# Optimization experiments

Hardware: AMD Instinct MI355X
Metric: run time of the kernel (lower is better)

The kernel has to match this reference:

```python
import jax, jax.numpy as jnp
import numpy as np

B, S, E, H, L, A = 4, 4096, 512, 8, 4, 3
NV, TD = 16, 6
WIN = 64
D = E // H
NEG = -1e9


def layer_norm(x, s, b):
    m = jnp.mean(x, axis=-1, keepdims=True)
    v = jnp.mean((x - m) ** 2, axis=-1, keepdims=True)
    return (x - m) * jax.lax.rsqrt(v + 1e-5) * s + b


def kmeans_attention(x, mask, Wq, Wk, Wv, Wo, means):
    # scatter-mean results back to sequence positions.
    b, n, e = x.shape
    split = lambda t: t.reshape(b, n, H, D).transpose(0, 2, 1, 3)  # (b,h,n,d)
    q, k, v = split(x @ Wq), split(x @ Wk), split(x @ Wv)
    qn = q / (jnp.linalg.norm(q, axis=-1, keepdims=True) + 1e-8)
    mn = means / (jnp.linalg.norm(means, axis=-1, keepdims=True) + 1e-8)
    dists = jnp.einsum('bhnd,hcd->bhcn', qn, mn)          # (b,h,C,n)
    _, idx = jax.lax.top_k(dists, WIN)                    # (b,h,C,w) token ids per cluster
    c = idx.shape[2]
    gather = lambda t: jnp.take_along_axis(t[:, :, None], idx[..., None], axis=3)
    qb, kb, vb = gather(q), gather(k), gather(v)          # (b,h,C,w,d)
    km = jnp.take_along_axis(jnp.broadcast_to(mask[:, None, None, :], (b, H, c, n)), idx, axis=3)
    scores = jnp.einsum('bhcwd,bhcxd->bhcwx', qb, kb) * (D ** -0.5)
    allowed = (idx[..., :, None] >= idx[..., None, :]) & km[..., None, :]
    attn = jax.nn.softmax(jnp.where(allowed, scores, NEG), axis=-1)
    ob = jnp.einsum('bhcwx,bhcxd->bhcwd', attn, vb)
    fi = idx.reshape(b, H, c * WIN)
    fo = ob.reshape(b, H, c * WIN, D)
    bi = jnp.arange(b)[:, None, None]
    hi = jnp.arange(H)[None, :, None]
    out = jnp.zeros((b, H, n, D), x.dtype).at[bi, hi, fi].add(fo)
    cnt = jnp.zeros((b, H, n), x.dtype).at[bi, hi, fi].add(1.0)
    out = out / jnp.maximum(cnt, 1.0)[..., None]          # scatter-mean
    return out.transpose(0, 2, 1, 3).reshape(b, n, e) @ Wo


def setup_inputs():
    key = jax.random.key(0)
    ks = jax.random.split(key, 20)
    w = lambda k, shp, s=0.02: jax.random.normal(k, shp, dtype=jnp.float32) * s
    return {
        'value': jax.random.randint(ks[0], (B, S), 0, NV + 1),
        'depth': jax.random.randint(ks[1], (B, S), 0, TD + 1),
        'pos': jax.random.randint(ks[2], (B, S, A), 0, 2 ** TD + 1),
        'sos': w(ks[3], (E,), 1.0),
        'tok_emb': w(ks[4], (NV + 1, E), 1.0).at[0].set(0.0),      # padding_idx=0
        'depth_emb': w(ks[5], (TD + 1, E), 1.0).at[0].set(0.0),
        'pos_emb': w(ks[6], (A, 2 ** TD + 1, E), 1.0).at[:, 0].set(0.0),
        'ln1_s': jnp.ones((L, E), jnp.float32),
        'ln1_b': jnp.zeros((L, E), jnp.float32),
        'Wq': w(ks[7], (L, E, E)),
        'Wk': w(ks[8], (L, E, E)),
        'Wv': w(ks[9], (L, E, E)),
        'Wo': w(ks[10], (L, E, E)),
        'means': w(ks[11], (L, H, S // WIN, D), 1.0),
        'ln2_s': jnp.ones((L, E), jnp.float32),
        'ln2_b': jnp.zeros((L, E), jnp.float32),
        'W1': w(ks[12], (L, E, 4 * E)),
        'b1': jnp.zeros((L, 4 * E), jnp.float32),
        'W2': w(ks[13], (L, 4 * E, E)),
        'b2': jnp.zeros((L, E), jnp.float32),
        'head_w': w(ks[14], (NV + 1, E)),
    }


def reference(value, depth, pos, sos, tok_emb, depth_emb, pos_emb, ln1_s, ln1_b, Wq, Wk, Wv, Wo, means, ln2_s, ln2_b, W1, b1, W2, b2, head_w):
    mask = value != 0
    x = tok_emb[value] + depth_emb[depth]
    for a in range(A):
        x = x + pos_emb[a][pos[:, :, a]]
    # shift right with learned sos token
    x = jnp.concatenate([jnp.broadcast_to(sos, (B, 1, E)), x[:, :-1]], axis=1)
    for l in range(L):
        h = layer_norm(x, ln1_s[l], ln1_b[l])
        x = x + kmeans_attention(h, mask, Wq[l], Wk[l], Wv[l], Wo[l], means[l])
        h = layer_norm(x, ln2_s[l], ln2_b[l])
        x = x + (jax.nn.gelu(h @ W1[l] + b1[l]) @ W2[l] + b2[l])
    return x @ head_w.T
```

## Files before the change

### kernel.cpp

```cpp
#include <hip/hip_runtime.h>
#include <hip/hip_bf16.h>
#include <math.h>

typedef __hip_bfloat16 bf16;
typedef __attribute__((ext_vector_type(2))) float f2v;
typedef __attribute__((ext_vector_type(8))) short bf16x8;
typedef __attribute__((ext_vector_type(4))) float f32x4;

#define NB 4
#define NS 4096
#define NE 512
#define NH 8
#define NL 4
#define NA 3
#define ND 64
#define NC 64
#define NW 64
#define NF 2048
#define NVOC 17
#define NTOK (NB * NS)

__device__ __forceinline__ float b2f(bf16 v) { return __bfloat162float(v); }
__device__ __forceinline__ float u2f(unsigned short u) { return __uint_as_float((unsigned)u << 16); }
__device__ __forceinline__ float ldw(const void* p, size_t i, int f32) {
  return f32 ? ((const float*)p)[i] : b2f(((const bf16*)p)[i]);
}
__device__ __forceinline__ unsigned short f2bf(float f) {
  unsigned u = __float_as_uint(f);
  return (unsigned short)((u + 0x7FFFu + ((u >> 16) & 1u)) >> 16);
}
__device__ __forceinline__ void split3(float a, unsigned short& h, unsigned short& m,
                                       unsigned short& l) {
  h = f2bf(a);
  float r = a - u2f(h);
  m = f2bf(r);
  float s = r - u2f(m);
  l = f2bf(s);
}

__global__ __launch_bounds__(256) void fill_out_kernel(float* __restrict__ out, int n, float val) {
  int i = blockIdx.x * 256 + threadIdx.x;
  if (i < n) out[i] = val;
}

__global__ __launch_bounds__(256) void zero_kernel(float* __restrict__ p, int n) {
  int i = blockIdx.x * 256 + threadIdx.x;
  if (i < n) p[i] = 0.f;
}

__global__ __launch_bounds__(256) void embed_kernel(
    const int* __restrict__ value, const int* __restrict__ depth, const int* __restrict__ pos,
    const void* __restrict__ sos, const void* __restrict__ tok_emb,
    const void* __restrict__ depth_emb, const void* __restrict__ pos_emb,
    float* __restrict__ x, int f32) {
  int i = blockIdx.x * 256 + threadIdx.x;
  if (i >= NTOK * NE) return;
  int e = i & (NE - 1);
  int bs = i >> 9;
  int s = bs & (NS - 1);
  int b = bs >> 12;
  float v;
  if (s == 0) {
    v = ldw(sos, e, f32);
  } else {
    int src = b * NS + (s - 1);
    float acc = ldw(tok_emb, (size_t)value[src] * NE + e, f32)
              + ldw(depth_emb, (size_t)depth[src] * NE + e, f32);
#pragma unroll
    for (int a = 0; a < NA; a++)
      acc += ldw(pos_emb, ((size_t)a * 65 + pos[src * NA + a]) * NE + e, f32);
    v = acc;
  }
  x[i] = v;
}

__global__ __launch_bounds__(256) void ln_kernel(
    const float* __restrict__ x, const void* __restrict__ gam, const void* __restrict__ bet,
    size_t off, float* __restrict__ out, int f32) {
  int row = blockIdx.x * 4 + (threadIdx.x >> 6);
  int lane = threadIdx.x & 63;
  const float* xr = x + (size_t)row * NE;
  float v[8];
#pragma unroll
  for (int i = 0; i < 8; i++) v[i] = xr[lane + i * 64];
  float s = 0.f;
#pragma unroll
  for (int i = 0; i < 8; i++) s += v[i];
#pragma unroll
  for (int o = 32; o; o >>= 1) s += __shfl_xor(s, o);
  float m = s * (1.0f / NE);
  float sq = 0.f;
#pragma unroll
  for (int i = 0; i < 8; i++) { float d = v[i] - m; sq += d * d; }
#pragma unroll
  for (int o = 32; o; o >>= 1) sq += __shfl_xor(sq, o);
  float rs = 1.0f / sqrtf(sq * (1.0f / NE) + 1e-5f);
  float* orow = out + (size_t)row * NE;
#pragma unroll
  for (int i = 0; i < 8; i++) {
    int e = lane + i * 64;
    orow[e] = (v[i] - m) * rs * ldw(gam, off + e, f32) + ldw(bet, off + e, f32);
  }
}

template <int ACT>
__device__ __forceinline__ void gemm_body(
    const float* __restrict__ A, const void* __restrict__ Bw, size_t bwoff, int ldb,
    const void* bias, size_t biasoff, const float* resid, float* C,
    int N, int K, int f32, int bm, int bn) {
  __shared__ float As[32][132];
  __shared__ float Bs[32][132];
  int tid = threadIdx.x;
  int ty = tid >> 4, tx = tid & 15;
  f2v acc2[8][4];
#pragma unroll
  for (int i = 0; i < 8; i++)
#pragma unroll
    for (int j = 0; j < 4; j++) acc2[i][j] = (f2v){0.f, 0.f};
  int arow = tid >> 1;
  int acol = (tid & 1) << 4;
  int brow = tid >> 3;
  int bcol = (tid & 7) << 4;

  const float* Aptr = A + (size_t)(bm + arow) * K + acol;
  float4 pa[4];
  float4 pb[4];
  uint4 pbu[2];
#pragma unroll
  for (int j = 0; j < 4; j++) pa[j] = *(const float4*)(Aptr + 4 * j);
  {
    size_t boff = bwoff + (size_t)brow * ldb + bn + bcol;
    if (f32) {
#pragma unroll
      for (int j = 0; j < 4; j++) pb[j] = *(const float4*)((const float*)Bw + boff + 4 * j);
    } else {
      pbu[0] = *(const uint4*)((const bf16*)Bw + boff);
      pbu[1] = *(const uint4*)((const bf16*)Bw + boff + 8);
    }
  }

  for (int k0 = 0; k0 < K; k0 += 32) {
#pragma unroll
    for (int j = 0; j < 4; j++) {
      As[acol + 4 * j + 0][arow] = pa[j].x;
      As[acol + 4 * j + 1][arow] = pa[j].y;
      As[acol + 4 * j + 2][arow] = pa[j].z;
      As[acol + 4 * j + 3][arow] = pa[j].w;
    }
    if (f32) {
#pragma unroll
      for (int j = 0; j < 4; j++) {
        Bs[brow][bcol + 4 * j + 0] = pb[j].x;
        Bs[brow][bcol + 4 * j + 1] = pb[j].y;
        Bs[brow][bcol + 4 * j + 2] = pb[j].z;
        Bs[brow][bcol + 4 * j + 3] = pb[j].w;
      }
    } else {
      union { uint4 u; unsigned short s[8]; } r0, r1;
      r0.u = pbu[0]; r1.u = pbu[1];
#pragma unroll
      for (int j = 0; j < 8; j++) Bs[brow][bcol + j] = u2f(r0.s[j]);
#pragma unroll
      for (int j = 0; j < 8; j++) Bs[brow][bcol + 8 + j] = u2f(r1.s[j]);
    }
    __syncthreads();
    if (k0 + 32 < K) {
#pragma unroll
      for (int j = 0; j < 4; j++) pa[j] = *(const float4*)(Aptr + k0 + 32 + 4 * j);
      size_t boff = bwoff + (size_t)(k0 + 32 + brow) * ldb + bn + bcol;
      if (f32) {
#pragma unroll
        for (int j = 0; j < 4; j++) pb[j] = *(const float4*)((const float*)Bw + boff + 4 * j);
      } else {
        pbu[0] = *(const uint4*)((const bf16*)Bw + boff);
        pbu[1] = *(const uint4*)((const bf16*)Bw + boff + 8);
      }
    }
#pragma unroll
    for (int kk = 0; kk < 32; kk++) {
      float4 aA = *(const float4*)&As[kk][ty << 3];
      float4 aB = *(const float4*)&As[kk][(ty << 3) + 4];
      float4 bA = *(const float4*)&Bs[kk][tx << 2];
      float4 bB = *(const float4*)&Bs[kk][64 + (tx << 2)];
      float av[8] = {aA.x, aA.y, aA.z, aA.w, aB.x, aB.y, aB.z, aB.w};
      f2v bv[4];
      bv[0] = (f2v){bA.x, bA.y};
      bv[1] = (f2v){bA.z, bA.w};
      bv[2] = (f2v){bB.x, bB.y};
      bv[3] = (f2v){bB.z, bB.w};
#pragma unroll
      for (int i = 0; i < 8; i++)
#pragma unroll
        for (int j = 0; j < 4; j++)
          acc2[i][j] += bv[j] * av[i];
    }
    __syncthreads();
  }
#pragma unroll
  for (int i = 0; i < 8; i++) {
    int row = bm + (ty << 3) + i;
    int c0 = bn + (tx << 2);
    int c1 = bn + 64 + (tx << 2);
    const float* ap = (const float*)&acc2[i][0];
    float o0[4], o1[4];
#pragma unroll
    for (int j = 0; j < 4; j++) { o0[j] = ap[j]; o1[j] = ap[4 + j]; }
    if (bias) {
#pragma unroll
      for (int j = 0; j < 4; j++) {
        o0[j] += ldw(bias, biasoff + c0 + j, f32);
        o1[j] += ldw(bias, biasoff + c1 + j, f32);
      }
    }
    if (ACT == 1) {
#pragma unroll
      for (int j = 0; j < 4; j++) {
        float t0 = 0.7978845608028654f * (o0[j] + 0.044715f * o0[j] * o0[j] * o0[j]);
        o0[j] = 0.5f * o0[j] * (1.0f + tanhf(t0));
        float t1 = 0.7978845608028654f * (o1[j] + 0.044715f * o1[j] * o1[j] * o1[j]);
        o1[j] = 0.5f * o1[j] * (1.0f + tanhf(t1));
      }
    }
    size_t p0 = (size_t)row * N + c0;
    size_t p1 = (size_t)row * N + c1;
    if (resid) {
      float4 r0 = *(const float4*)(resid + p0);
      float4 r1 = *(const float4*)(resid + p1);
      o0[0] += r0.x; o0[1] += r0.y; o0[2] += r0.z; o0[3] += r0.w;
      o1[0] += r1.x; o1[1] += r1.y; o1[2] += r1.z; o1[3] += r1.w;
    }
    *(float4*)(C + p0) = make_float4(o0[0], o0[1], o0[2], o0[3]);
    *(float4*)(C + p1) = make_float4(o1[0], o1[1], o1[2], o1[3]);
  }
}

template <int ACT>
__global__ __launch_bounds__(256) void gemm_kernel(
    const float* __restrict__ A, const void* __restrict__ Bw, size_t bwoff, int ldb,
    const void* bias, size_t biasoff, const float* resid, float* C,
    int N, int K, int f32) {
  gemm_body<ACT>(A, Bw, bwoff, ldb, bias, biasoff, resid, C, N, K,
                 f32, blockIdx.y << 7, blockIdx.x << 7);
}

__global__ __launch_bounds__(256) void gemm_qkv_kernel(
    const float* __restrict__ A,
    const void* __restrict__ Wq, const void* __restrict__ Wk, const void* __restrict__ Wv,
    size_t bwoff, float* __restrict__ Cq, float* __restrict__ Ck, float* __restrict__ Cv,
    int f32) {
  int sel = blockIdx.x >> 2;
  const void* Bw = (sel == 0) ? Wq : ((sel == 1) ? Wk : Wv);
  float* C = (sel == 0) ? Cq : ((sel == 1) ? Ck : Cv);
  gemm_body<0>(A, Bw, bwoff, NE, nullptr, 0, nullptr, C, NE, NE,
               f32, blockIdx.y << 7, (blockIdx.x & 3) << 7);
}

template <int ACT, int FULL>
__device__ __forceinline__ void mfma_body(
    const float* __restrict__ A, const float* __restrict__ Bw, int ldb,
    const float* __restrict__ bias, const float* __restrict__ resid, float* __restrict__ C,
    int N, int K, int bm, int bn) {
  __shared__ unsigned short Ah[128][40];
  __shared__ unsigned short Am[128][40];
  __shared__ unsigned short Al[FULL ? 128 : 1][40];
  __shared__ unsigned short Bh[128][40];
  __shared__ unsigned short Bm[128][40];
  __shared__ unsigned short Bl[FULL ? 128 : 1][40];
  int t = threadIdx.x;
  int arow = t >> 1;
  int akc = (t & 1) << 4;
  const float* Ap = A + (size_t)(bm + arow) * K + akc;
  int bkr = t >> 3;
  int bcg = t & 7;
  const float* Bp = Bw + (size_t)bkr * ldb + bn + bcg * 16;
  int bkpos = bkr ^ ((bcg & 3) << 3);

  float4 pa[4], pb[4];
#pragma unroll
  for (int j = 0; j < 4; j++) pa[j] = *(const float4*)(Ap + 4 * j);
#pragma unroll
  for (int j = 0; j < 4; j++) pb[j] = *(const float4*)(Bp + 4 * j);

  int lane = t & 63;
  int wid = t >> 6;
  int wr = wid >> 1, wc = wid & 1;
  int lr = lane & 15, lg = lane >> 4;

  f32x4 acc[4][4];
#pragma unroll
  for (int i = 0; i < 4; i++)
#pragma unroll
    for (int j = 0; j < 4; j++) acc[i][j] = (f32x4){0.f, 0.f, 0.f, 0.f};

  for (int k0 = 0; k0 < K; k0 += 32) {
    {
      unsigned hs[8], ms[8], ls[8];
#pragma unroll
      for (int j = 0; j < 4; j++) {
        const float* pf = (const float*)&pa[j];
#pragma unroll
        for (int e = 0; e < 2; e++) {
          float a0 = pf[2 * e], a1 = pf[2 * e + 1];
          unsigned short h0 = f2bf(a0), h1 = f2bf(a1);
          float r0 = a0 - u2f(h0), r1 = a1 - u2f(h1);
          unsigned short m0 = f2bf(r0), m1 = f2bf(r1);
          hs[2 * j + e] = (unsigned)h0 | ((unsigned)h1 << 16);
          ms[2 * j + e] = (unsigned)m0 | ((unsigned)m1 << 16);
          if (FULL) {
            float s0 = r0 - u2f(m0), s1 = r1 - u2f(m1);
            unsigned short l0 = f2bf(s0), l1 = f2bf(s1);
            ls[2 * j + e] = (unsigned)l0 | ((unsigned)l1 << 16);
          }
        }
      }
      *(uint4*)&Ah[arow][akc]     = make_uint4(hs[0], hs[1], hs[2], hs[3]);
      *(uint4*)&Ah[arow][akc + 8] = make_uint4(hs[4], hs[5], hs[6], hs[7]);
      *(uint4*)&Am[arow][akc]     = make_uint4(ms[0], ms[1], ms[2], ms[3]);
      *(uint4*)&Am[arow][akc + 8] = make_uint4(ms[4], ms[5], ms[6], ms[7]);
      if (FULL) {
        *(uint4*)&Al[arow][akc]     = make_uint4(ls[0], ls[1], ls[2], ls[3]);
        *(uint4*)&Al[arow][akc + 8] = make_uint4(ls[4], ls[5], ls[6], ls[7]);
      }
    }
    {
#pragma unroll
      for (int j = 0; j < 4; j++) {
        const float* pf = (const float*)&pb[j];
#pragma unroll
        for (int e = 0; e < 4; e++) {
          float a = pf[e];
          unsigned short h = f2bf(a);
          float r = a - u2f(h);
          unsigned short m = f2bf(r);
          int nn = bcg * 16 + 4 * j + e;
          Bh[nn][bkpos] = h;
          Bm[nn][bkpos] = m;
          if (FULL) {
            float s = r - u2f(m);
            Bl[nn][bkpos] = f2bf(s);
          }
        }
      }
    }
    __syncthreads();
    if (k0 + 32 < K) {
#pragma unroll
      for (int j = 0; j < 4; j++) pa[j] = *(const float4*)(Ap + k0 + 32 + 4 * j);
      const float* Bn = Bp + (size_t)(k0 + 32) * ldb;
#pragma unroll
      for (int j = 0; j < 4; j++) pb[j] = *(const float4*)(Bn + 4 * j);
    }
    bf16x8 fbh[4], fbm[4], fbl[4];
#pragma unroll
    for (int ni = 0; ni < 4; ni++) {
      int rb = wc * 64 + ni * 16 + lr;
      int cb = ((lg ^ ni) & 3) * 8;
      fbh[ni] = *(const bf16x8*)&Bh[rb][cb];
      fbm[ni] = *(const bf16x8*)&Bm[rb][cb];
      if (FULL) fbl[ni] = *(const bf16x8*)&Bl[rb][cb];
    }
#pragma unroll
    for (int mi = 0; mi < 4; mi++) {
      int ar = wr * 64 + mi * 16 + lr;
      bf16x8 fh = *(const bf16x8*)&Ah[ar][lg * 8];
      bf16x8 fm = *(const bf16x8*)&Am[ar][lg * 8];
      bf16x8 fl;
      if (FULL) fl = *(const bf16x8*)&Al[ar][lg * 8];
#pragma unroll
      for (int ni = 0; ni < 4; ni++) {
        f32x4 a = acc[mi][ni];
        a = __builtin_amdgcn_mfma_f32_16x16x32_bf16(fh, fbh[ni], a, 0, 0, 0);
        a = __builtin_amdgcn_mfma_f32_16x16x32_bf16(fh, fbm[ni], a, 0, 0, 0);
        a = __builtin_amdgcn_mfma_f32_16x16x32_bf16(fm, fbh[ni], a, 0, 0, 0);
        if (FULL) {
          a = __builtin_amdgcn_mfma_f32_16x16x32_bf16(fm, fbm[ni], a, 0, 0, 0);
          a = __builtin_amdgcn_mfma_f32_16x16x32_bf16(fh, fbl[ni], a, 0, 0, 0);
          a = __builtin_amdgcn_mfma_f32_16x16x32_bf16(fl, fbh[ni], a, 0, 0, 0);
        }
        acc[mi][ni] = a;
      }
    }
    __syncthreads();
  }
#pragma unroll
  for (int mi = 0; mi < 4; mi++) {
#pragma unroll
    for (int ni = 0; ni < 4; ni++) {
      int col = bn + wc * 64 + ni * 16 + lr;
      int rbase = bm + wr * 64 + mi * 16 + lg * 4;
      float bv = bias ? bias[col] : 0.f;
      const float* av = (const float*)&acc[mi][ni];
#pragma unroll
      for (int r = 0; r < 4; r++) {
        float o = av[r] + bv;
        if (ACT == 1) {
          float t0 = 0.7978845608028654f * (o + 0.044715f * o * o * o);
          o = 0.5f * o * (1.0f + tanhf(t0));
        }
        size_t p = (size_t)(rbase + r) * N + col;
        if (resid) o += resid[p];
        C[p] = o;
      }
    }
  }
}

template <int ACT, int FULL>
__global__ __launch_bounds__(256) void gemm_mfma_kernel(
    const float* __restrict__ A, const float* __restrict__ Bw, int ldb,
    const float* __restrict__ bias, const float* __restrict__ resid, float* __restrict__ C,
    int N, int K) {
  mfma_body<ACT, FULL>(A, Bw, ldb, bias, resid, C, N, K, blockIdx.y << 7, blockIdx.x << 7);
}

__global__ __launch_bounds__(256) void gemm_kv_mfma(
    const float* __restrict__ A, const float* __restrict__ Wk, const float* __restrict__ Wv,
    size_t off, float* __restrict__ Ck, float* __restrict__ Cv) {
  int sel = blockIdx.x >> 2;
  const float* Bw = sel ? Wv : Wk;
  float* C = sel ? Cv : Ck;
  mfma_body<0, 0>(A, Bw + off, NE, nullptr, nullptr, C, NE, NE,
                  blockIdx.y << 7, (blockIdx.x & 3) << 7);
}

__global__ __launch_bounds__(256) void qt_kernel(const float* __restrict__ q, float* __restrict__ qT,
                                                 double* __restrict__ rqd) {
  __shared__ float tile[64][65];
  int bid = blockIdx.x;
  int st = bid & 63;
  int bh = bid >> 6;
  int b = bh >> 3, h = bh & 7;
  int s0 = st * 64;
  int t = threadIdx.x;
#pragma unroll
  for (int k = 0; k < 16; k++) {
    int idx = t + k * 256;
    int sl = idx >> 6, dl = idx & 63;
    tile[sl][dl] = q[(size_t)(b * NS + s0 + sl) * NE + h * ND + dl];
  }
  __syncthreads();
#pragma unroll
  for (int k = 0; k < 16; k++) {
    int idx = t + k * 256;
    int dl = idx >> 6, sl = idx & 63;
    qT[((size_t)bh * 64 + dl) * NS + s0 + sl] = tile[sl][dl];
  }
  int w = t >> 6, lane = t & 63;
#pragma unroll
  for (int i = 0; i < 16; i++) {
    int tok = w * 16 + i;
    double v = (double)tile[tok][lane];
    double ss = v * v;
#pragma unroll
    for (int o = 32; o; o >>= 1) ss += __shfl_xor(ss, o);
    if (lane == 0) rqd[((size_t)bh << 12) | (s0 + tok)] = 1.0 / (sqrt(ss) + 1e-8);
  }
}

__global__ __launch_bounds__(64) void mnd_kernel(const void* __restrict__ means,
                                                 double* __restrict__ mnd, int f32) {
  __shared__ double s[64];
  int vblk = blockIdx.x;
  int d = threadIdx.x;
  double m = (double)ldw(means, (size_t)vblk * ND + d, f32);
  s[d] = m * m;
  __syncthreads();
  for (int st = 32; st; st >>= 1) { if (d < st) s[d] += s[d + st]; __syncthreads(); }
  mnd[(size_t)vblk * ND + d] = m / (sqrt(s[0]) + 1e-8);
}

__global__ __launch_bounds__(256) void route_kernel(
    const float* __restrict__ qT, const double* __restrict__ mnd,
    const double* __restrict__ rqd, int* __restrict__ idxout, float* __restrict__ cnt) {
  __shared__ unsigned long long keys[NS];
  __shared__ double mc[ND];
  __shared__ unsigned hist[256];
  __shared__ unsigned short cand[2][NS];
  __shared__ unsigned s_rem, s_cnt, s_sel, s_cc[2];
  int bid = blockIdx.x;
  int h = bid & 7;
  int b = (bid >> 3) & 3;
  int c = bid >> 5;
  int bhc = ((b * NH + h) * NC) + c;
  int t = threadIdx.x;
  if (t < ND) mc[t] = mnd[((size_t)h * NC + c) * ND + t];
  hist[t] = 0u;
  if (t == 0) { s_rem = NW; s_cnt = 0u; s_cc[0] = 0u; s_cc[1] = 0u; }
  __syncthreads();
  const float* qTb = qT + (size_t)(b * NH + h) * 64 * NS;
  const double* rqb = rqd + ((size_t)(b * NH + h) << 12);
  for (int i = 0; i < 16; i += 4) {
    int n0 = t + i * 256, n1 = n0 + 256, n2 = n0 + 512, n3 = n0 + 768;
    double a0 = 0.0, a1 = 0.0, a2 = 0.0, a3 = 0.0;
#pragma unroll 8
    for (int d = 0; d < 64; d++) {
      const float* row = qTb + (size_t)d * NS;
      double m = mc[d];
      a0 += (double)row[n0] * m;
      a1 += (double)row[n1] * m;
      a2 += (double)row[n2] * m;
      a3 += (double)row[n3] * m;
    }
    double dv[4] = {a0 * rqb[n0], a1 * rqb[n1], a2 * rqb[n2], a3 * rqb[n3]};
    int nn[4] = {n0, n1, n2, n3};
#pragma unroll
    for (int j = 0; j < 4; j++) {
      long long sb = __double_as_longlong(dv[j]);
      unsigned long long u = (unsigned long long)sb;
      u = (sb < 0) ? ~u : (u | 0x8000000000000000ULL);
      keys[nn[j]] = (u & 0xFFFFFFFFFFFFF000ULL) | (unsigned long long)(NS - 1 - nn[j]);
    }
  }
  __syncthreads();
  {
    unsigned lastd = 0xFFFFFFFFu, lcnt = 0u;
    for (int n = t; n < NS; n += 256) {
      unsigned d = (unsigned)(keys[n] >> 56);
      if (d == lastd) { lcnt++; }
      else { if (lcnt) atomicAdd(&hist[lastd], lcnt); lastd = d; lcnt = 1u; }
    }
    if (lcnt) atomicAdd(&hist[lastd], lcnt);
  }
  __syncthreads();
  if (t < 64) {
    unsigned h0 = hist[4 * t + 0], h1 = hist[4 * t + 1];
    unsigned h2 = hist[4 * t + 2], h3 = hist[4 * t + 3];
    hist[4 * t + 0] = 0u; hist[4 * t + 1] = 0u; hist[4 * t + 2] = 0u; hist[4 * t + 3] = 0u;
    unsigned t3 = h3, t2 = h2 + h3, t1 = h1 + t2, t0 = h0 + t1;
    unsigned s = t0;
#pragma unroll
    for (int off = 1; off < 64; off <<= 1) {
      unsigned v = __shfl_down(s, off);
      if (t + off < 64) s += v;
    }
    unsigned E = s - t0;
    unsigned rem = s_rem;
    unsigned sf0 = t0 + E, sf1 = t1 + E, sf2 = t2 + E, sf3 = t3 + E, sf4 = E;
    if (sf0 >= rem && sf1 < rem) { s_sel = 4u * t + 0u; s_rem = rem - sf1; }
    if (sf1 >= rem && sf2 < rem) { s_sel = 4u * t + 1u; s_rem = rem - sf2; }
    if (sf2 >= rem && sf3 < rem) { s_sel = 4u * t + 2u; s_rem = rem - sf3; }
    if (sf3 >= rem && sf4 < rem) { s_sel = 4u * t + 3u; s_rem = rem - sf4; }
  }
  __syncthreads();
  {
    unsigned sel = s_sel;
    for (int n = t; n < NS; n += 256) {
      unsigned d = (unsigned)(keys[n] >> 56);
      if (d > sel) {
        unsigned p = atomicAdd(&s_cnt, 1u);
        idxout[(size_t)bhc * NW + p] = n;
        atomicAdd(&cnt[(size_t)(b * NS + n) * NH + h], 1.0f);
      } else if (d == sel) {
        unsigned p = atomicAdd(&s_cc[0], 1u);
        cand[0][p] = (unsigned short)n;
      }
    }
  }
  __syncthreads();
  int cur = 0;
  for (int p = 6; p >= 0; p--) {
    int sh = p * 8;
    unsigned nc = s_cc[cur];
    for (unsigned i = t; i < nc; i += 256) {
      unsigned d = (unsigned)((keys[cand[cur][i]] >> sh) & 255ULL);
      atomicAdd(&hist[d], 1u);
    }
    __syncthreads();
    if (t < 64) {
      unsigned h0 = hist[4 * t + 0], h1 = hist[4 * t + 1];
      unsigned h2 = hist[4 * t + 2], h3 = hist[4 * t + 3];
      hist[4 * t + 0] = 0u; hist[4 * t + 1] = 0u; hist[4 * t + 2] = 0u; hist[4 * t + 3] = 0u;
      unsigned t3 = h3, t2 = h2 + h3, t1 = h1 + t2, t0 = h0 + t1;
      unsigned s = t0;
#pragma unroll
      for (int off = 1; off < 64; off <<= 1) {
        unsigned v = __shfl_down(s, off);
        if (t + off < 64) s += v;
      }
      unsigned E = s - t0;
      unsigned rem = s_rem;
      unsigned sf0 = t0 + E, sf1 = t1 + E, sf2 = t2 + E, sf3 = t3 + E, sf4 = E;
      if (sf0 >= rem && sf1 < rem) { s_sel = 4u * t + 0u; s_rem = rem - sf1; }
      if (sf1 >= rem && sf2 < rem) { s_sel = 4u * t + 1u; s_rem = rem - sf2; }
      if (sf2 >= rem && sf3 < rem) { s_sel = 4u * t + 2u; s_rem = rem - sf3; }
      if (sf3 >= rem && sf4 < rem) { s_sel = 4u * t + 3u; s_rem = rem - sf4; }
      if (t == 0) s_cc[cur ^ 1] = 0u;
    }
    __syncthreads();
    unsigned sel = s_sel;
    if (p == 0) {
      for (unsigned i = t; i < nc; i += 256) {
        unsigned n = cand[cur][i];
        unsigned d = (unsigned)(keys[n] & 255ULL);
        if (d >= sel) {
          unsigned pp = atomicAdd(&s_cnt, 1u);
          idxout[(size_t)bhc * NW + pp] = n;
          atomicAdd(&cnt[(size_t)(b * NS + n) * NH + h], 1.0f);
        }
      }
    } else {
      int nxt = cur ^ 1;
      for (unsigned i = t; i < nc; i += 256) {
        unsigned n = cand[cur][i];
        unsigned d = (unsigned)((keys[n] >> sh) & 255ULL);
        if (d > sel) {
          unsigned pp = atomicAdd(&s_cnt, 1u);
          idxout[(size_t)bhc * NW + pp] = n;
          atomicAdd(&cnt[(size_t)(b * NS + n) * NH + h], 1.0f);
        } else if (d == sel) {
          unsigned pp = atomicAdd(&s_cc[nxt], 1u);
          cand[nxt][pp] = (unsigned short)n;
        }
      }
      __syncthreads();
      cur = nxt;
    }
  }
}

__global__ __launch_bounds__(256) void attn_kernel(
    const float* __restrict__ q, const float* __restrict__ k, const float* __restrict__ v,
    const int* __restrict__ idxb, const int* __restrict__ value, const float* __restrict__ cnt,
    float* __restrict__ obuf) {
  __shared__ float qs[NW * (ND + 1)];
  __shared__ float ks[NW * (ND + 1)];
  __shared__ float sc[NW * (NW + 1)];
  __shared__ int idxs[NW];
  __shared__ float kmv[NW];
  __shared__ float cinv[NW];
  int bhc = blockIdx.x;
  int h = (bhc >> 6) & (NH - 1);
  int b = bhc >> 9;
  int t = threadIdx.x;
  if (t < NW) {
    int n = idxb[(size_t)bhc * NW + t];
    idxs[t] = n;
    kmv[t] = (value[b * NS + n] != 0) ? 1.f : 0.f;
    cinv[t] = 1.0f / fmaxf(cnt[(size_t)(b * NS + n) * NH + h], 1.0f);
  }
  __syncthreads();
  for (int p = t; p < NW * ND; p += 256) {
    int w = p >> 6, d = p & (ND - 1);
    size_t src = (size_t)(b * NS + idxs[w]) * NE + h * ND + d;
    qs[w * (ND + 1) + d] = q[src];
    ks[w * (ND + 1) + d] = k[src];
  }
  __syncthreads();
  for (int p = t; p < NW * NW; p += 256) {
    int w = p >> 6, x = p & (NW - 1);
    float dot = 0.f;
#pragma unroll 16
    for (int d = 0; d < ND; d++) dot += qs[w * (ND + 1) + d] * ks[x * (ND + 1) + d];
    bool allowed = (idxs[w] >= idxs[x]) && (kmv[x] != 0.f);
    sc[w * (NW + 1) + x] = allowed ? dot * 0.125f : -1e9f;
  }
  __syncthreads();
  if (t < NW) {
    float mx = -3.4e38f;
    for (int x = 0; x < NW; x++) mx = fmaxf(mx, sc[t * (NW + 1) + x]);
    float sum = 0.f;
    for (int x = 0; x < NW; x++) {
      float e = expf(sc[t * (NW + 1) + x] - mx);
      sc[t * (NW + 1) + x] = e;
      sum += e;
    }
    float inv = cinv[t] / sum;
    for (int x = 0; x < NW; x++) sc[t * (NW + 1) + x] *= inv;
  }
  for (int p = t; p < NW * ND; p += 256) {
    int w = p >> 6, d = p & (ND - 1);
    ks[w * (ND + 1) + d] = v[(size_t)(b * NS + idxs[w]) * NE + h * ND + d];
  }
  __syncthreads();
  for (int p = t; p < NW * ND; p += 256) {
    int w = p >> 6, d = p & (ND - 1);
    float o = 0.f;
#pragma unroll 16
    for (int x = 0; x < NW; x++) o += sc[w * (NW + 1) + x] * ks[x * (ND + 1) + d];
    qs[w * (ND + 1) + d] = o;
  }
  __syncthreads();
  for (int p = t; p < NW * ND; p += 256) {
    int w = p >> 6, d = p & (ND - 1);
    atomicAdd(&obuf[(size_t)(b * NS + idxs[w]) * NE + h * ND + d], qs[w * (ND + 1) + d]);
  }
}

__global__ __launch_bounds__(256) void head_kernel(
    const float* __restrict__ x, const void* __restrict__ hw, void* __restrict__ out, int f32) {
  int gw = (blockIdx.x * 256 + threadIdx.x) >> 6;
  int lane = threadIdx.x & 63;
  if (gw >= NTOK * NVOC) return;
  int row = gw / NVOC, vv = gw % NVOC;
  const float* xr = x + (size_t)row * NE;
  float acc = 0.f;
  for (int e = lane; e < NE; e += 64) acc += xr[e] * ldw(hw, (size_t)vv * NE + e, f32);
#pragma unroll
  for (int o = 32; o; o >>= 1) acc += __shfl_down(acc, o);
  if (lane == 0) {
    if (f32) ((float*)out)[(size_t)row * NVOC + vv] = acc;
    else ((bf16*)out)[(size_t)row * NVOC + vv] = __float2bfloat16(acc);
  }
}

extern "C" void kernel_launch(void* const* d_in, const int* in_sizes, int n_in,
                              void* d_out, int out_size, void* d_ws, size_t ws_size,
                              hipStream_t stream) {
  const int* value = (const int*)d_in[0];
  const int* depth = (const int*)d_in[1];
  const int* pos = (const int*)d_in[2];
  const void* sos = d_in[3];
  const void* tok_emb = d_in[4];
  const void* depth_emb = d_in[5];
  const void* pos_emb = d_in[6];
  const void* ln1_s = d_in[7];
  const void* ln1_b = d_in[8];
  const void* Wq = d_in[9];
  const void* Wk = d_in[10];
  const void* Wv = d_in[11];
  const void* Wo = d_in[12];
  const void* means = d_in[13];
  const void* ln2_s = d_in[14];
  const void* ln2_b = d_in[15];
  const void* W1 = d_in[16];
  const void* b1 = d_in[17];
  const void* W2 = d_in[18];
  const void* b2 = d_in[19];
  const void* head_w = d_in[20];
  (void)n_in;

  int f32 = (in_sizes[4] != 17408) ? 1 : 0;

  const size_t NX = (size_t)NTOK * NE;
  const size_t NEED = 170917896ULL;
  if (ws_size < NEED) {
    float val = (float)(unsigned)(ws_size >> 20) * 1000.0f;
    fill_out_kernel<<<(out_size + 255) / 256, 256, 0, stream>>>((float*)d_out, out_size, val);
    return;
  }

  float* xbuf = (float*)d_ws;
  float* hbuf = xbuf + NX;
  float* qbuf = hbuf + NX;
  float* kbuf = qbuf + NX;
  float* vbuf = kbuf + NX;
  double* mndbuf = (double*)(vbuf + NX);
  double* rqdbuf = mndbuf + (size_t)NL * NH * NC * ND;
  float* cntbuf = (float*)(rqdbuf + (size_t)NTOK * NH);
  int* idxbuf = (int*)(cntbuf + (size_t)NTOK * NH);
  float* mid = kbuf;

  mnd_kernel<<<NL * NH * NC, 64, 0, stream>>>(means, mndbuf, f32);
  embed_kernel<<<(int)((NX + 255) / 256), 256, 0, stream>>>(
      value, depth, pos, sos, tok_emb, depth_emb, pos_emb, xbuf, f32);

  dim3 g512(NE / 128, NTOK / 128);
  dim3 gkv(8, NTOK / 128);

  if (f32) {
    const float* Wqf = (const float*)Wq;
    const float* Wkf = (const float*)Wk;
    const float* Wvf = (const float*)Wv;
    const float* Wof = (const float*)Wo;
    const float* W1f = (const float*)W1;
    const float* W2f = (const float*)W2;
    const float* b1f = (const float*)b1;
    const float* b2f = (const float*)b2;
    for (int l = 0; l < NL; l++) {
      size_t o_w = (size_t)l * NE * NE;
      size_t o_w1 = (size_t)l * NE * NF;
      size_t o_w2 = (size_t)l * NF * NE;
      size_t o_e = (size_t)l * NE;
      size_t o_f = (size_t)l * NF;

      ln_kernel<<<NTOK / 4, 256, 0, stream>>>(xbuf, ln1_s, ln1_b, o_e, hbuf, 1);
      gemm_mfma_kernel<0, 1><<<g512, 256, 0, stream>>>(hbuf, Wqf + o_w, NE, nullptr, nullptr,
                                                       qbuf, NE, NE);
      gemm_kv_mfma<<<gkv, 256, 0, stream>>>(hbuf, Wkf, Wvf, o_w, kbuf, vbuf);

      qt_kernel<<<NB * NH * 64, 256, 0, stream>>>(qbuf, hbuf, rqdbuf);
      zero_kernel<<<(NTOK * NH) / 256, 256, 0, stream>>>(cntbuf, NTOK * NH);
      route_kernel<<<NB * NH * NC, 256, 0, stream>>>(
          hbuf, mndbuf + (size_t)l * NH * NC * ND, rqdbuf, idxbuf, cntbuf);

      zero_kernel<<<(int)((NX + 255) / 256), 256, 0, stream>>>(hbuf, (int)NX);
      attn_kernel<<<NB * NH * NC, 256, 0, stream>>>(qbuf, kbuf, vbuf, idxbuf, value, cntbuf, hbuf);
      gemm_mfma_kernel<0, 0><<<g512, 256, 0, stream>>>(hbuf, Wof + o_w, NE, nullptr, xbuf,
                                                       xbuf, NE, NE);

      ln_kernel<<<NTOK / 4, 256, 0, stream>>>(xbuf, ln2_s, ln2_b, o_e, qbuf, 1);
      for (int c = 0; c < 4; c++) {
        gemm_mfma_kernel<1, 0><<<g512, 256, 0, stream>>>(
            qbuf, W1f + o_w1 + (size_t)c * 512, NF, b1f + o_f + (size_t)c * 512,
            nullptr, mid, 512, NE);
        gemm_mfma_kernel<0, 0><<<g512, 256, 0, stream>>>(
            mid, W2f + o_w2 + (size_t)c * 512 * NE, NE,
            (c == 0) ? (b2f + o_e) : nullptr, xbuf, xbuf, NE, 512);
      }
    }
  } else {
    const int CH = 8192;
    dim3 gqkvv(12, NTOK / 128);
    dim3 gW1(NF / 128, CH / 128);
    dim3 gW2(NE / 128, CH / 128);
    for (int l = 0; l < NL; l++) {
      size_t o_w = (size_t)l * NE * NE;
      size_t o_w1 = (size_t)l * NE * NF;
      size_t o_w2 = (size_t)l * NF * NE;
      size_t o_e = (size_t)l * NE;
      size_t o_f = (size_t)l * NF;

      ln_kernel<<<NTOK / 4, 256, 0, stream>>>(xbuf, ln1_s, ln1_b, o_e, hbuf, 0);
      gemm_qkv_kernel<<<gqkvv, 256, 0, stream>>>(hbuf, Wq, Wk, Wv, o_w, qbuf, kbuf, vbuf, 0);

      qt_kernel<<<NB * NH * 64, 256, 0, stream>>>(qbuf, hbuf, rqdbuf);
      zero_kernel<<<(NTOK * NH) / 256, 256, 0, stream>>>(cntbuf, NTOK * NH);
      route_kernel<<<NB * NH * NC, 256, 0, stream>>>(
          hbuf, mndbuf + (size_t)l * NH * NC * ND, rqdbuf, idxbuf, cntbuf);

      zero_kernel<<<(int)((NX + 255) / 256), 256, 0, stream>>>(hbuf, (int)NX);
      attn_kernel<<<NB * NH * NC, 256, 0, stream>>>(qbuf, kbuf, vbuf, idxbuf, value, cntbuf, hbuf);
      gemm_kernel<0><<<g512, 256, 0, stream>>>(hbuf, Wo, o_w, NE, nullptr, 0, xbuf,
                                               xbuf, NE, NE, 0);

      ln_kernel<<<NTOK / 4, 256, 0, stream>>>(xbuf, ln2_s, ln2_b, o_e, qbuf, 0);
      for (int ch = 0; ch < NTOK / CH; ch++) {
        const float* hch = qbuf + (size_t)ch * CH * NE;
        float* xch = xbuf + (size_t)ch * CH * NE;
        gemm_kernel<1><<<gW1, 256, 0, stream>>>(hch, W1, o_w1, NF, b1, o_f, nullptr,
                                                mid, NF, NE, 0);
        gemm_kernel<0><<<gW2, 256, 0, stream>>>(mid, W2, o_w2, NE, b2, o_e, xch,
                                                xch, NE, NF, 0);
      }
    }
  }

  head_kernel<<<(NTOK * NVOC * 64 + 255) / 256, 256, 0, stream>>>(xbuf, head_w, d_out, f32);
}
```

Measured before the change: 3.972 ms.

## Vectorize bucket attention smem access and restructure FFN into token-chunked full-width GEMMs

The attention kernel now pads shared rows to 68 floats and uses float4 loads for the gathers, the QK dot products and the PV accumulation. This cuts LDS instruction count and global load transactions. The f32 FFN path drops the four hidden-dimension chunks, which needed eight small GEMM launches per layer, and instead runs full-width W1 and W2 GEMMs over two 8192-token chunks. This gives larger grids, fewer launches and a single bias add, at the cost of a larger intermediate buffer held in kbuf. The f32 split3 helper is also removed as dead code.

```diff
diff --git a/kernel.cpp b/kernel.cpp
--- a/kernel.cpp
+++ b/kernel.cpp
@@ -19,6 +19,7 @@
 #define NF 2048
 #define NVOC 17
 #define NTOK (NB * NS)
+#define AP 68
 
 __device__ __forceinline__ float b2f(bf16 v) { return __bfloat162float(v); }
 __device__ __forceinline__ float u2f(unsigned short u) { return __uint_as_float((unsigned)u << 16); }
@@ -28,14 +29,6 @@
 __device__ __forceinline__ unsigned short f2bf(float f) {
   unsigned u = __float_as_uint(f);
   return (unsigned short)((u + 0x7FFFu + ((u >> 16) & 1u)) >> 16);
-}
-__device__ __forceinline__ void split3(float a, unsigned short& h, unsigned short& m,
-                                       unsigned short& l) {
-  h = f2bf(a);
-  float r = a - u2f(h);
-  m = f2bf(r);
-  float s = r - u2f(m);
-  l = f2bf(s);
 }
 
 __global__ __launch_bounds__(256) void fill_out_kernel(float* __restrict__ out, int n, float val) {
@@ -622,9 +615,9 @@
     const float* __restrict__ q, const float* __restrict__ k, const float* __restrict__ v,
     const int* __restrict__ idxb, const int* __restrict__ value, const float* __restrict__ cnt,
     float* __restrict__ obuf) {
-  __shared__ float qs[NW * (ND + 1)];
-  __shared__ float ks[NW * (ND + 1)];
-  __shared__ float sc[NW * (NW + 1)];
+  __shared__ float qs[NW * AP];
+  __shared__ float ks[NW * AP];
+  __shared__ float sc[NW * AP];
   __shared__ int idxs[NW];
   __shared__ float kmv[NW];
   __shared__ float cinv[NW];
@@ -639,50 +632,73 @@
     cinv[t] = 1.0f / fmaxf(cnt[(size_t)(b * NS + n) * NH + h], 1.0f);
   }
   __syncthreads();
+#pragma unroll
+  for (int j = 0; j < 4; j++) {
+    int p = t + j * 256;
+    int w = p >> 4, d4 = p & 15;
+    size_t src = (size_t)(b * NS + idxs[w]) * NE + h * ND + 4 * d4;
+    *(float4*)&qs[w * AP + 4 * d4] = *(const float4*)(q + src);
+    *(float4*)&ks[w * AP + 4 * d4] = *(const float4*)(k + src);
+  }
+  __syncthreads();
+#pragma unroll
+  for (int j = 0; j < 16; j++) {
+    int p = t + j * 256;
+    int w = p >> 6, x = p & (NW - 1);
+    float dot = 0.f;
+#pragma unroll
+    for (int i = 0; i < 16; i++) {
+      float4 a = *(const float4*)&qs[w * AP + 4 * i];
+      float4 bb = *(const float4*)&ks[x * AP + 4 * i];
+      dot += a.x * bb.x;
+      dot += a.y * bb.y;
+      dot += a.z * bb.z;
+      dot += a.w * bb.w;
+    }
+    bool allowed = (idxs[w] >= idxs[x]) && (kmv[x] != 0.f);
+    sc[w * AP + x] = allowed ? dot * 0.125f : -1e9f;
+  }
+  __syncthreads();
+  if (t < NW) {
+    float mx = -3.4e38f;
+    for (int x = 0; x < NW; x++) mx = fmaxf(mx, sc[t * AP + x]);
+    float sum = 0.f;
+    for (int x = 0; x < NW; x++) {
+      float e = expf(sc[t * AP + x] - mx);
+      sc[t * AP + x] = e;
+      sum += e;
+    }
+    float inv = cinv[t] / sum;
+    for (int x = 0; x < NW; x++) sc[t * AP + x] *= inv;
+  }
+  __syncthreads();
+#pragma unroll
+  for (int j = 0; j < 4; j++) {
+    int p = t + j * 256;
+    int w = p >> 4, d4 = p & 15;
+    size_t src = (size_t)(b * NS + idxs[w]) * NE + h * ND + 4 * d4;
+    *(float4*)&ks[w * AP + 4 * d4] = *(const float4*)(v + src);
+  }
+  __syncthreads();
+#pragma unroll
+  for (int j = 0; j < 4; j++) {
+    int p = t + j * 256;
+    int w = p >> 4, d4 = p & 15;
+    float4 o4 = make_float4(0.f, 0.f, 0.f, 0.f);
+    for (int x = 0; x < NW; x++) {
+      float s = sc[w * AP + x];
+      float4 kv = *(const float4*)&ks[x * AP + 4 * d4];
+      o4.x += s * kv.x;
+      o4.y += s * kv.y;
+      o4.z += s * kv.z;
+      o4.w += s * kv.w;
+    }
+    *(float4*)&qs[w * AP + 4 * d4] = o4;
+  }
+  __syncthreads();
   for (int p = t; p < NW * ND; p += 256) {
     int w = p >> 6, d = p & (ND - 1);
-    size_t src = (size_t)(b * NS + idxs[w]) * NE + h * ND + d;
-    qs[w * (ND + 1) + d] = q[src];
-    ks[w * (ND + 1) + d] = k[src];
-  }
-  __syncthreads();
-  for (int p = t; p < NW * NW; p += 256) {
-    int w = p >> 6, x = p & (NW - 1);
-    float dot = 0.f;
-#pragma unroll 16
-    for (int d = 0; d < ND; d++) dot += qs[w * (ND + 1) + d] * ks[x * (ND + 1) + d];
-    bool allowed = (idxs[w] >= idxs[x]) && (kmv[x] != 0.f);
-    sc[w * (NW + 1) + x] = allowed ? dot * 0.125f : -1e9f;
-  }
-  __syncthreads();
-  if (t < NW) {
-    float mx = -3.4e38f;
-    for (int x = 0; x < NW; x++) mx = fmaxf(mx, sc[t * (NW + 1) + x]);
-    float sum = 0.f;
-    for (int x = 0; x < NW; x++) {
-      float e = expf(sc[t * (NW + 1) + x] - mx);
-      sc[t * (NW + 1) + x] = e;
-      sum += e;
-    }
-    float inv = cinv[t] / sum;
-    for (int x = 0; x < NW; x++) sc[t * (NW + 1) + x] *= inv;
-  }
-  for (int p = t; p < NW * ND; p += 256) {
-    int w = p >> 6, d = p & (ND - 1);
-    ks[w * (ND + 1) + d] = v[(size_t)(b * NS + idxs[w]) * NE + h * ND + d];
-  }
-  __syncthreads();
-  for (int p = t; p < NW * ND; p += 256) {
-    int w = p >> 6, d = p & (ND - 1);
-    float o = 0.f;
-#pragma unroll 16
-    for (int x = 0; x < NW; x++) o += sc[w * (NW + 1) + x] * ks[x * (ND + 1) + d];
-    qs[w * (ND + 1) + d] = o;
-  }
-  __syncthreads();
-  for (int p = t; p < NW * ND; p += 256) {
-    int w = p >> 6, d = p & (ND - 1);
-    atomicAdd(&obuf[(size_t)(b * NS + idxs[w]) * NE + h * ND + d], qs[w * (ND + 1) + d]);
+    atomicAdd(&obuf[(size_t)(b * NS + idxs[w]) * NE + h * ND + d], qs[w * AP + d]);
   }
 }
 
@@ -756,6 +772,9 @@
 
   dim3 g512(NE / 128, NTOK / 128);
   dim3 gkv(8, NTOK / 128);
+  const int CH = 8192;
+  dim3 gW1(NF / 128, CH / 128);
+  dim3 gW2(NE / 128, CH / 128);
 
   if (f32) {
     const float* Wqf = (const float*)Wq;
@@ -789,20 +808,17 @@
                                                        xbuf, NE, NE);
 
       ln_kernel<<<NTOK / 4, 256, 0, stream>>>(xbuf, ln2_s, ln2_b, o_e, qbuf, 1);
-      for (int c = 0; c < 4; c++) {
-        gemm_mfma_kernel<1, 0><<<g512, 256, 0, stream>>>(
-            qbuf, W1f + o_w1 + (size_t)c * 512, NF, b1f + o_f + (size_t)c * 512,
-            nullptr, mid, 512, NE);
-        gemm_mfma_kernel<0, 0><<<g512, 256, 0, stream>>>(
-            mid, W2f + o_w2 + (size_t)c * 512 * NE, NE,
-            (c == 0) ? (b2f + o_e) : nullptr, xbuf, xbuf, NE, 512);
+      for (int mc = 0; mc < NTOK / CH; mc++) {
+        const float* hch = qbuf + (size_t)mc * CH * NE;
+        float* xch = xbuf + (size_t)mc * CH * NE;
+        gemm_mfma_kernel<1, 0><<<gW1, 256, 0, stream>>>(hch, W1f + o_w1, NF, b1f + o_f,
+                                                        nullptr, mid, NF, NE);
+        gemm_mfma_kernel<0, 0><<<gW2, 256, 0, stream>>>(mid, W2f + o_w2, NE, b2f + o_e,
+                                                        xch, xch, NE, NF);
       }
     }
   } else {
-    const int CH = 8192;
     dim3 gqkvv(12, NTOK / 128);
-    dim3 gW1(NF / 128, CH / 128);
-    dim3 gW2(NE / 128, CH / 128);
     for (int l = 0; l < NL; l++) {
       size_t o_w = (size_t)l * NE * NE;
       size_t o_w1 = (size_t)l * NE * NF;
```

After: 3.786 ms. 4.7% less time.
